# Performance work log

Hardware: AMD Instinct MI355X
Metric: run time of the kernel (lower is better)

The kernel has to match this reference:

```python
import jax, jax.numpy as jnp
import numpy as np

B, C, H, W_ = 4, 256, 64, 64
INTER = 128

def conv1x1(x, w, b):
    # x: [B,C,H,W], w: [O,C], b: [O] -> [B,O,H,W]
    return jnp.einsum('bchw,oc->bohw', x, w) + b[None, :, None, None]

def setup_inputs() -> dict:
    key = jax.random.key(0)
    ks = jax.random.split(key, 5)
    s_in = 1.0 / np.sqrt(C)
    s_mid = 1.0 / np.sqrt(INTER)
    return {
        'x': jax.random.normal(ks[0], (B, C, H, W_), dtype=jnp.float32),
        'w_g': jax.random.normal(ks[1], (INTER, C), dtype=jnp.float32) * s_in,
        'b_g': jnp.zeros((INTER,), dtype=jnp.float32),
        'w_theta': jax.random.normal(ks[2], (INTER, C), dtype=jnp.float32) * s_in,
        'b_theta': jnp.zeros((INTER,), dtype=jnp.float32),
        'w_phi': jax.random.normal(ks[3], (INTER, C), dtype=jnp.float32) * s_in,
        'b_phi': jnp.zeros((INTER,), dtype=jnp.float32),
        'w_out': jax.random.normal(ks[4], (C, INTER), dtype=jnp.float32) * s_mid,
        'b_out': jnp.zeros((C,), dtype=jnp.float32),
    }

def reference(x, w_g, b_g, w_theta, b_theta, w_phi, b_phi, w_out, b_out):
    b, c, h, w = x.shape
    n = h * w
    # 1x1 conv projections, flatten spatial dims to N tokens
    g_x = conv1x1(x, w_g, b_g).reshape(b, INTER, n).transpose(0, 2, 1)      # [B,N,I]
    theta_x = conv1x1(x, w_theta, b_theta).reshape(b, INTER, n).transpose(0, 2, 1)  # [B,N,I]
    phi_x = conv1x1(x, w_phi, b_phi).reshape(b, INTER, n)                   # [B,I,N]
    f = jnp.einsum('bni,bim->bnm', theta_x, phi_x)                          # [B,N,N]
    f_div_C = jax.nn.softmax(f, axis=-1)
    y = jnp.einsum('bnm,bmi->bni', f_div_C, g_x)                            # [B,N,I]
    y = y.transpose(0, 2, 1).reshape(b, INTER, h, w)
    W_y = conv1x1(y, w_out, b_out)                                          # [B,C,H,W]
    return W_y + x
```

## Files before the change

kernel.cpp:

```cpp
#include <hip/hip_runtime.h>

#define BB 4
#define CC 256
#define NN 4096
#define II 128
#define LOG2E 1.4426950408889634f

typedef float f32x4 __attribute__((ext_vector_type(4)));
typedef _Float16 f16x8 __attribute__((ext_vector_type(8)));

static __device__ __forceinline__ unsigned short f2h(float f) {
    _Float16 h = (_Float16)f;
    return __builtin_bit_cast(unsigned short, h);
}
static __device__ __forceinline__ float h2f(unsigned short s) {
    return (float)__builtin_bit_cast(_Float16, s);
}
static __device__ __forceinline__ unsigned int pack2h(float a, float b) {
    return (unsigned int)f2h(a) | ((unsigned int)f2h(b) << 16);
}
static __device__ __forceinline__ unsigned int cvt2h(float a, float b) {
    return __builtin_bit_cast(unsigned int, __builtin_amdgcn_cvt_pkrtz(a, b));
}
#define M3(a, b, c) fmaxf(fmaxf((a), (b)), (c))

__global__ __launch_bounds__(256) void proj_kernel(
    const float* __restrict__ x,
    const float* __restrict__ w_th, const float* __restrict__ b_th,
    const float* __restrict__ w_ph, const float* __restrict__ b_ph,
    const float* __restrict__ w_g,  const float* __restrict__ b_g,
    const float* __restrict__ w_out,
    unsigned short* __restrict__ Qb, unsigned short* __restrict__ Kb,
    unsigned short* __restrict__ Vt, unsigned short* __restrict__ Wo)
{
    __shared__ char lds[57344];
    unsigned short* xl = (unsigned short*)lds;

    int tid = threadIdx.x;
    int w = tid >> 6, l = tid & 63, g = l >> 4, cl = l & 15;
    int b = blockIdx.y, n0 = blockIdx.x * 64;
    const float* wp0 = w_th; const float* wp1 = w_ph; const float* wp2 = w_g;

    f32x4 acc[3][2][4];
    #pragma unroll
    for (int m = 0; m < 3; ++m)
        #pragma unroll
        for (int it = 0; it < 2; ++it)
            #pragma unroll
            for (int nt = 0; nt < 4; ++nt) acc[m][it][nt] = (f32x4){0.f, 0.f, 0.f, 0.f};

    const float* xb = x + (size_t)b * CC * NN;
    int c2 = tid >> 3, nch = tid & 7;

    for (int c0 = 0; c0 < CC; c0 += 64) {
        __syncthreads();
        {
            const float* xsrc = xb + (size_t)(c0 + c2 * 2) * NN + n0 + nch * 8;
            float4 x00 = *(const float4*)xsrc;
            float4 x01 = *(const float4*)(xsrc + 4);
            float4 x10 = *(const float4*)(xsrc + NN);
            float4 x11 = *(const float4*)(xsrc + NN + 4);
            float lo[8] = {x00.x, x00.y, x00.z, x00.w, x01.x, x01.y, x01.z, x01.w};
            float hi[8] = {x10.x, x10.y, x10.z, x10.w, x11.x, x11.y, x11.z, x11.w};
            #pragma unroll
            for (int t = 0; t < 8; ++t) {
                int n = nch * 8 + t;
                *(unsigned int*)((char*)xl + n * 128 + ((c2 * 4) ^ ((n & 7) << 4))) = pack2h(lo[t], hi[t]);
            }
        }
        #pragma unroll
        for (int r = 0; r < 12; ++r) {
            const int mat = r >> 2;
            int ir = (r & 3) * 32 + (tid >> 3), ch = tid & 7;
            const float* wsrc = (mat == 0 ? wp0 : mat == 1 ? wp1 : wp2) + ir * CC + c0 + ch * 8;
            float4 a = *(const float4*)wsrc;
            float4 bq = *(const float4*)(wsrc + 4);
            union { unsigned int u[4]; uint4 q; } pk;
            pk.u[0] = pack2h(a.x, a.y);   pk.u[1] = pack2h(a.z, a.w);
            pk.u[2] = pack2h(bq.x, bq.y); pk.u[3] = pack2h(bq.z, bq.w);
            *(uint4*)(lds + 8192 + mat * 16384 + ir * 128 + ((ch ^ (ir & 7)) << 4)) = pk.q;
        }
        __syncthreads();
        #pragma unroll
        for (int kc = 0; kc < 2; ++kc) {
            f16x8 bf[4];
            #pragma unroll
            for (int nt = 0; nt < 4; ++nt) {
                int row = nt * 16 + cl;
                bf[nt] = *(const f16x8*)((const char*)xl + row * 128 + (((kc * 4 + g) ^ (row & 7)) << 4));
            }
            #pragma unroll
            for (int m = 0; m < 3; ++m) {
                f16x8 af[2];
                #pragma unroll
                for (int it = 0; it < 2; ++it) {
                    int row = w * 32 + it * 16 + cl;
                    af[it] = *(const f16x8*)(lds + 8192 + m * 16384 + row * 128 + (((kc * 4 + g) ^ (row & 7)) << 4));
                }
                #pragma unroll
                for (int it = 0; it < 2; ++it)
                    #pragma unroll
                    for (int nt = 0; nt < 4; ++nt)
                        acc[m][it][nt] = __builtin_amdgcn_mfma_f32_16x16x32_f16(af[it], bf[nt], acc[m][it][nt], 0, 0, 0);
            }
        }
    }

    float bv[3][2][4];
    #pragma unroll
    for (int m = 0; m < 3; ++m) {
        const float* bp = (m == 0) ? b_th : (m == 1) ? b_ph : b_g;
        #pragma unroll
        for (int it = 0; it < 2; ++it)
            #pragma unroll
            for (int r = 0; r < 4; ++r) bv[m][it][r] = bp[w * 32 + it * 16 + 4 * g + r];
    }

    #pragma unroll
    for (int m = 0; m < 2; ++m) {
        float scale = (m == 0) ? LOG2E : 1.0f;
        unsigned short* pk = (unsigned short*)lds;
        __syncthreads();
        #pragma unroll
        for (int it = 0; it < 2; ++it)
            #pragma unroll
            for (int nt = 0; nt < 4; ++nt)
                #pragma unroll
                for (int r = 0; r < 4; r += 2) {
                    int n = nt * 16 + cl;
                    int i = w * 32 + it * 16 + 4 * g + r;
                    unsigned int v = pack2h((acc[m][it][nt][r] + bv[m][it][r]) * scale,
                                            (acc[m][it][nt][r + 1] + bv[m][it][r + 1]) * scale);
                    *(unsigned int*)((char*)pk + n * 256 + ((i * 2) ^ ((n & 7) << 4))) = v;
                }
        __syncthreads();
        unsigned short* out = (m == 0) ? Qb : Kb;
        #pragma unroll
        for (int r = 0; r < 4; ++r) {
            int idx = r * 256 + tid;
            int n = idx >> 4, seg = idx & 15;
            uint4 q = *(const uint4*)((const char*)pk + n * 256 + ((seg << 4) ^ ((n & 7) << 4)));
            *(uint4*)(out + (size_t)(b * NN + n0 + n) * II + seg * 8) = q;
        }
    }
    {
        unsigned short* pk = (unsigned short*)lds;
        __syncthreads();
        #pragma unroll
        for (int it = 0; it < 2; ++it)
            #pragma unroll
            for (int nt = 0; nt < 4; ++nt)
                #pragma unroll
                for (int r = 0; r < 4; ++r) {
                    int i = w * 32 + it * 16 + 4 * g + r;
                    int n = nt * 16 + cl;
                    *(unsigned short*)((char*)pk + i * 128 + ((n * 2) ^ ((i & 7) << 4))) =
                        f2h(acc[2][it][nt][r] + bv[2][it][r]);
                }
        __syncthreads();
        #pragma unroll
        for (int r = 0; r < 4; ++r) {
            int idx = r * 256 + tid;
            int i = idx >> 3, seg = idx & 7;
            uint4 q = *(const uint4*)((const char*)pk + i * 128 + ((seg << 4) ^ ((i & 7) << 4)));
            *(uint4*)(Vt + (size_t)(b * II + i) * NN + n0 + seg * 8) = q;
        }
    }
    if (blockIdx.x == 0 && b == 0) {
        #pragma unroll
        for (int r = 0; r < 16; ++r) {
            int idx = (r * 256 + tid) * 8;
            float4 a = *(const float4*)(w_out + idx);
            float4 b4 = *(const float4*)(w_out + idx + 4);
            union { unsigned int u[4]; uint4 q; } pw;
            pw.u[0] = pack2h(a.x, a.y);   pw.u[1] = pack2h(a.z, a.w);
            pw.u[2] = pack2h(b4.x, b4.y); pw.u[3] = pack2h(b4.z, b4.w);
            *(uint4*)&Wo[idx] = pw.q;
        }
    }
}

template<int NS>
__global__ __launch_bounds__(256, 2) void attn_kernel(
    const unsigned short* __restrict__ Qb,
    const unsigned short* __restrict__ Kb,
    const unsigned short* __restrict__ Vb,
    unsigned short* __restrict__ Yp,
    float2* __restrict__ ML)
{
    constexpr int KVH = NN / NS;
    constexpr int NT = KVH / 64;
    constexpr int HALF = NS / 2;
    constexpr int QSH = (NS == 8) ? 5 : 4;

    __shared__ unsigned short Ks[64 * 128];
    __shared__ unsigned short Vs[128 * 64];

    int tid = threadIdx.x;
    int w = tid >> 6, l = tid & 63, g = l >> 4, cl = l & 15;
    int id = blockIdx.x;
    int comb = (id & 7) * HALF + ((id >> 3) & (HALF - 1));
    int b = comb / NS, sp = comb % NS, qt = id >> QSH;
    int qr0 = qt * 128;
    int m_base = sp * KVH;

    f16x8 qa0[4], qa1[4];
    {
        const unsigned short* qrow0 = Qb + (size_t)(b * NN + qr0 + w * 32 + cl) * II;
        const unsigned short* qrow1 = qrow0 + 16 * II;
        #pragma unroll
        for (int kc = 0; kc < 4; ++kc) {
            qa0[kc] = *(const f16x8*)(qrow0 + kc * 32 + g * 8);
            qa1[kc] = *(const f16x8*)(qrow1 + kc * 32 + g * 8);
        }
    }
    const f16x8 onesv = {(_Float16)1.f, (_Float16)1.f, (_Float16)1.f, (_Float16)1.f,
                         (_Float16)1.f, (_Float16)1.f, (_Float16)1.f, (_Float16)1.f};

    f32x4 yacc0[8], yacc1[8], lacc0, lacc1;
    #pragma unroll
    for (int it = 0; it < 8; ++it) {
        yacc0[it] = (f32x4){0.f, 0.f, 0.f, 0.f};
        yacc1[it] = (f32x4){0.f, 0.f, 0.f, 0.f};
    }
    lacc0 = (f32x4){0.f, 0.f, 0.f, 0.f};
    lacc1 = (f32x4){0.f, 0.f, 0.f, 0.f};
    float mrun0 = -1e30f, mrun1 = -1e30f;

    const unsigned short* kb = Kb + (size_t)(b * NN + m_base) * II;
    const unsigned short* vb = Vb + (size_t)b * II * NN + m_base;
    int krow = tid >> 4, kch = tid & 15;
    int vrow = tid >> 3, vch = tid & 7;
    int kswz = (kch ^ (krow & 7)) << 4;
    int vsw = (vrow & 7) << 4;
    int vc0 = ((vch >> 2) * 32 + (vch & 1) * 16 + ((vch >> 1) & 1) * 4) * 2;

    uint4 k0, k1, k2, k3, v0, v1, v2, v3;
    k0 = *(const uint4*)(kb + (size_t)(krow) * II + kch * 8);
    k1 = *(const uint4*)(kb + (size_t)(16 + krow) * II + kch * 8);
    k2 = *(const uint4*)(kb + (size_t)(32 + krow) * II + kch * 8);
    k3 = *(const uint4*)(kb + (size_t)(48 + krow) * II + kch * 8);
    v0 = *(const uint4*)(vb + (size_t)(vrow) * NN + vch * 8);
    v1 = *(const uint4*)(vb + (size_t)(32 + vrow) * NN + vch * 8);
    v2 = *(const uint4*)(vb + (size_t)(64 + vrow) * NN + vch * 8);
    v3 = *(const uint4*)(vb + (size_t)(96 + vrow) * NN + vch * 8);

    for (int t = 0; t < NT; ++t) {
        __syncthreads();
        *(uint4*)((char*)Ks + (krow) * 256 + kswz) = k0;
        *(uint4*)((char*)Ks + (16 + krow) * 256 + kswz) = k1;
        *(uint4*)((char*)Ks + (32 + krow) * 256 + kswz) = k2;
        *(uint4*)((char*)Ks + (48 + krow) * 256 + kswz) = k3;
        {
            uint2 lo, hi;
            lo.x = v0.x; lo.y = v0.y; hi.x = v0.z; hi.y = v0.w;
            *(uint2*)((char*)Vs + (vrow) * 128 + (vc0 ^ vsw)) = lo;
            *(uint2*)((char*)Vs + (vrow) * 128 + ((vc0 + 16) ^ vsw)) = hi;
            lo.x = v1.x; lo.y = v1.y; hi.x = v1.z; hi.y = v1.w;
            *(uint2*)((char*)Vs + (32 + vrow) * 128 + (vc0 ^ vsw)) = lo;
            *(uint2*)((char*)Vs + (32 + vrow) * 128 + ((vc0 + 16) ^ vsw)) = hi;
            lo.x = v2.x; lo.y = v2.y; hi.x = v2.z; hi.y = v2.w;
            *(uint2*)((char*)Vs + (64 + vrow) * 128 + (vc0 ^ vsw)) = lo;
            *(uint2*)((char*)Vs + (64 + vrow) * 128 + ((vc0 + 16) ^ vsw)) = hi;
            lo.x = v3.x; lo.y = v3.y; hi.x = v3.z; hi.y = v3.w;
            *(uint2*)((char*)Vs + (96 + vrow) * 128 + (vc0 ^ vsw)) = lo;
            *(uint2*)((char*)Vs + (96 + vrow) * 128 + ((vc0 + 16) ^ vsw)) = hi;
        }
        __syncthreads();
        if (t + 1 < NT) {
            const unsigned short* kp = kb + (size_t)(t + 1) * 64 * II;
            k0 = *(const uint4*)(kp + (size_t)(krow) * II + kch * 8);
            k1 = *(const uint4*)(kp + (size_t)(16 + krow) * II + kch * 8);
            k2 = *(const uint4*)(kp + (size_t)(32 + krow) * II + kch * 8);
            k3 = *(const uint4*)(kp + (size_t)(48 + krow) * II + kch * 8);
        }

        f32x4 s0[4], s1[4];
        #pragma unroll
        for (int mt = 0; mt < 4; ++mt) {
            s0[mt] = (f32x4){0.f, 0.f, 0.f, 0.f};
            s1[mt] = (f32x4){0.f, 0.f, 0.f, 0.f};
        }
        __builtin_amdgcn_s_setprio(1);
        #pragma unroll
        for (int mt = 0; mt < 4; ++mt) {
            int row = mt * 16 + cl;
            #pragma unroll
            for (int kc = 0; kc < 4; ++kc) {
                f16x8 kf = *(const f16x8*)((const char*)Ks + row * 256 + (((kc * 4 + g) ^ (row & 7)) << 4));
                s0[mt] = __builtin_amdgcn_mfma_f32_16x16x32_f16(kf, qa0[kc], s0[mt], 0, 0, 0);
                s1[mt] = __builtin_amdgcn_mfma_f32_16x16x32_f16(kf, qa1[kc], s1[mt], 0, 0, 0);
            }
        }
        __builtin_amdgcn_s_setprio(0);
        if (t + 1 < NT) {
            const unsigned short* vp = vb + (size_t)(t + 1) * 64;
            v0 = *(const uint4*)(vp + (size_t)(vrow) * NN + vch * 8);
            v1 = *(const uint4*)(vp + (size_t)(32 + vrow) * NN + vch * 8);
            v2 = *(const uint4*)(vp + (size_t)(64 + vrow) * NN + vch * 8);
            v3 = *(const uint4*)(vp + (size_t)(96 + vrow) * NN + vch * 8);
        }

        union { unsigned int u[4]; f16x8 v; } pb00, pb01, pb10, pb11;
        {
            float t0 = M3(s0[0][0], s0[0][1], s0[0][2]);
            float t1 = M3(s0[0][3], s0[1][0], s0[1][1]);
            float t2 = M3(s0[1][2], s0[1][3], s0[2][0]);
            float t3 = M3(s0[2][1], s0[2][2], s0[2][3]);
            float t4 = M3(s0[3][0], s0[3][1], s0[3][2]);
            float tmax = fmaxf(M3(t0, t1, t2), M3(t3, t4, s0[3][3]));
            tmax = fmaxf(tmax, __shfl_xor(tmax, 16));
            tmax = fmaxf(tmax, __shfl_xor(tmax, 32));
            if (!__all(tmax <= mrun0 + 8.0f)) {
                float mnew = fmaxf(mrun0, tmax);
                float corr = exp2f(mrun0 - mnew);
                mrun0 = mnew;
                #pragma unroll
                for (int it = 0; it < 8; ++it)
                    #pragma unroll
                    for (int r = 0; r < 4; ++r) yacc0[it][r] *= corr;
                #pragma unroll
                for (int r = 0; r < 4; ++r) lacc0[r] *= corr;
            }
            #pragma unroll
            for (int mt = 0; mt < 4; ++mt) {
                unsigned int ua = cvt2h(exp2f(s0[mt][0] - mrun0), exp2f(s0[mt][1] - mrun0));
                unsigned int ub = cvt2h(exp2f(s0[mt][2] - mrun0), exp2f(s0[mt][3] - mrun0));
                if (mt < 2) { pb00.u[mt * 2] = ua; pb00.u[mt * 2 + 1] = ub; }
                else        { pb01.u[(mt - 2) * 2] = ua; pb01.u[(mt - 2) * 2 + 1] = ub; }
            }
        }
        {
            float t0 = M3(s1[0][0], s1[0][1], s1[0][2]);
            float t1 = M3(s1[0][3], s1[1][0], s1[1][1]);
            float t2 = M3(s1[1][2], s1[1][3], s1[2][0]);
            float t3 = M3(s1[2][1], s1[2][2], s1[2][3]);
            float t4 = M3(s1[3][0], s1[3][1], s1[3][2]);
            float tmax = fmaxf(M3(t0, t1, t2), M3(t3, t4, s1[3][3]));
            tmax = fmaxf(tmax, __shfl_xor(tmax, 16));
            tmax = fmaxf(tmax, __shfl_xor(tmax, 32));
            if (!__all(tmax <= mrun1 + 8.0f)) {
                float mnew = fmaxf(mrun1, tmax);
                float corr = exp2f(mrun1 - mnew);
                mrun1 = mnew;
                #pragma unroll
                for (int it = 0; it < 8; ++it)
                    #pragma unroll
                    for (int r = 0; r < 4; ++r) yacc1[it][r] *= corr;
                #pragma unroll
                for (int r = 0; r < 4; ++r) lacc1[r] *= corr;
            }
            #pragma unroll
            for (int mt = 0; mt < 4; ++mt) {
                unsigned int ua = cvt2h(exp2f(s1[mt][0] - mrun1), exp2f(s1[mt][1] - mrun1));
                unsigned int ub = cvt2h(exp2f(s1[mt][2] - mrun1), exp2f(s1[mt][3] - mrun1));
                if (mt < 2) { pb10.u[mt * 2] = ua; pb10.u[mt * 2 + 1] = ub; }
                else        { pb11.u[(mt - 2) * 2] = ua; pb11.u[(mt - 2) * 2 + 1] = ub; }
            }
        }

        __builtin_amdgcn_s_setprio(1);
        lacc0 = __builtin_amdgcn_mfma_f32_16x16x32_f16(onesv, pb00.v, lacc0, 0, 0, 0);
        lacc0 = __builtin_amdgcn_mfma_f32_16x16x32_f16(onesv, pb01.v, lacc0, 0, 0, 0);
        lacc1 = __builtin_amdgcn_mfma_f32_16x16x32_f16(onesv, pb10.v, lacc1, 0, 0, 0);
        lacc1 = __builtin_amdgcn_mfma_f32_16x16x32_f16(onesv, pb11.v, lacc1, 0, 0, 0);
        #pragma unroll
        for (int it = 0; it < 8; ++it) {
            int row = it * 16 + cl;
            f16x8 vf0 = *(const f16x8*)((const char*)Vs + row * 128 + ((g ^ (row & 7)) << 4));
            f16x8 vf1 = *(const f16x8*)((const char*)Vs + row * 128 + (((4 + g) ^ (row & 7)) << 4));
            yacc0[it] = __builtin_amdgcn_mfma_f32_16x16x32_f16(vf0, pb00.v, yacc0[it], 0, 0, 0);
            yacc0[it] = __builtin_amdgcn_mfma_f32_16x16x32_f16(vf1, pb01.v, yacc0[it], 0, 0, 0);
            yacc1[it] = __builtin_amdgcn_mfma_f32_16x16x32_f16(vf0, pb10.v, yacc1[it], 0, 0, 0);
            yacc1[it] = __builtin_amdgcn_mfma_f32_16x16x32_f16(vf1, pb11.v, yacc1[it], 0, 0, 0);
        }
        __builtin_amdgcn_s_setprio(0);
    }

    __syncthreads();

    unsigned short* ys = Ks + w * 2048;
    size_t rowbase0 = (size_t)((sp * BB + b) * NN + qr0 + w * 32);
    int prow = l >> 2;
    {
        float rl = 1.0f / lacc0[0];
        #pragma unroll
        for (int it = 0; it < 8; ++it)
            #pragma unroll
            for (int r = 0; r < 4; r += 2) {
                int i = it * 16 + 4 * g + r;
                *(unsigned int*)((char*)ys + cl * 256 + ((i * 2) ^ ((cl & 7) << 4))) =
                    pack2h(yacc0[it][r] * rl, yacc0[it][r + 1] * rl);
            }
        #pragma unroll
        for (int c = 0; c < 4; ++c) {
            int seg = c * 4 + (l & 3);
            uint4 q = *(const uint4*)((const char*)ys + prow * 256 + ((seg << 4) ^ ((prow & 7) << 4)));
            *(uint4*)(Yp + (rowbase0 + prow) * II + seg * 8) = q;
        }
    }
    {
        float rl = 1.0f / lacc1[0];
        #pragma unroll
        for (int it = 0; it < 8; ++it)
            #pragma unroll
            for (int r = 0; r < 4; r += 2) {
                int i = it * 16 + 4 * g + r;
                *(unsigned int*)((char*)ys + cl * 256 + ((i * 2) ^ ((cl & 7) << 4))) =
                    pack2h(yacc1[it][r] * rl, yacc1[it][r + 1] * rl);
            }
        #pragma unroll
        for (int c = 0; c < 4; ++c) {
            int seg = c * 4 + (l & 3);
            uint4 q = *(const uint4*)((const char*)ys + prow * 256 + ((seg << 4) ^ ((prow & 7) << 4)));
            *(uint4*)(Yp + (rowbase0 + 16 + prow) * II + seg * 8) = q;
        }
    }
    if (l < 16) {
        float2 v; v.x = mrun0; v.y = lacc0[0];
        ML[rowbase0 + l] = v;
    } else if (l < 32) {
        float2 v; v.x = mrun1; v.y = lacc1[0];
        ML[rowbase0 + 16 + (l - 16)] = v;
    }
}

template<int NS>
__global__ __launch_bounds__(256) void combine_kernel(
    const unsigned short* __restrict__ Yp, const float2* __restrict__ ML,
    const unsigned short* __restrict__ Wo, const float* __restrict__ b_out,
    const float* __restrict__ x, float* __restrict__ out)
{
    __shared__ unsigned short Ys[4][16 * 128];

    int tid = threadIdx.x;
    int w = tid >> 6, l = tid & 63, g = l >> 4, cl = l & 15;
    int qt = blockIdx.x, b = blockIdx.y;
    int qr0 = qt * 64;
    int n = qr0 + w * 16 + cl;

    float ms[NS], ls[NS], wgt[NS];
    float M = -1e30f;
    #pragma unroll
    for (int s = 0; s < NS; ++s) {
        float2 ml = ML[(size_t)(s * BB + b) * NN + n];
        ms[s] = ml.x; ls[s] = ml.y;
        M = fmaxf(M, ml.x);
    }
    float wsum = 0.f;
    #pragma unroll
    for (int s = 0; s < NS; ++s) { wgt[s] = exp2f(ms[s] - M) * ls[s]; wsum += wgt[s]; }
    float rd = 1.0f / wsum;
    #pragma unroll
    for (int s = 0; s < NS; ++s) wgt[s] *= rd;

    unsigned short* ys = Ys[w];
    #pragma unroll
    for (int j = 0; j < 4; ++j) {
        float acc[8];
        #pragma unroll
        for (int e = 0; e < 8; ++e) acc[e] = 0.f;
        #pragma unroll
        for (int s = 0; s < NS; ++s) {
            union { unsigned short s16[8]; uint4 q; } a;
            a.q = *(const uint4*)(Yp + ((size_t)(s * BB + b) * NN + n) * II + g * 32 + j * 8);
            #pragma unroll
            for (int e = 0; e < 8; ++e) acc[e] += wgt[s] * h2f(a.s16[e]);
        }
        union { unsigned int u[4]; uint4 q; } o;
        #pragma unroll
        for (int e = 0; e < 4; ++e) o.u[e] = pack2h(acc[e * 2], acc[e * 2 + 1]);
        *(uint4*)((char*)ys + cl * 256 + (((g * 4 + j) ^ (cl & 7)) << 4)) = o.q;
    }

    f32x4 zero4 = {0.f, 0.f, 0.f, 0.f};
    f16x8 yf[4];
    #pragma unroll
    for (int kc = 0; kc < 4; ++kc)
        yf[kc] = *(const f16x8*)((const char*)ys + cl * 256 + (((kc * 4 + g) ^ (cl & 7)) << 4));
    for (int ct = 0; ct < 16; ++ct) {
        f32x4 oa = zero4;
        #pragma unroll
        for (int kc = 0; kc < 4; ++kc) {
            f16x8 wf = *(const f16x8*)(Wo + (ct * 16 + cl) * II + kc * 32 + g * 8);
            oa = __builtin_amdgcn_mfma_f32_16x16x32_f16(wf, yf[kc], oa, 0, 0, 0);
        }
        #pragma unroll
        for (int r = 0; r < 4; ++r) {
            int c = ct * 16 + 4 * g + r;
            size_t off = (size_t)(b * CC + c) * NN + n;
            out[off] = oa[r] + b_out[c] + x[off];
        }
    }
}

extern "C" void kernel_launch(void* const* d_in, const int* in_sizes, int n_in,
                              void* d_out, int out_size, void* d_ws, size_t ws_size,
                              hipStream_t stream) {
    const float* x     = (const float*)d_in[0];
    const float* w_g   = (const float*)d_in[1];
    const float* b_g   = (const float*)d_in[2];
    const float* w_th  = (const float*)d_in[3];
    const float* b_th  = (const float*)d_in[4];
    const float* w_ph  = (const float*)d_in[5];
    const float* b_ph  = (const float*)d_in[6];
    const float* w_out = (const float*)d_in[7];
    const float* b_o   = (const float*)d_in[8];
    float* out = (float*)d_out;

    const size_t SZ = (size_t)BB * NN * II;
    unsigned short* Qb = (unsigned short*)d_ws;
    unsigned short* Kb = Qb + SZ;
    unsigned short* Vt = Kb + SZ;
    unsigned short* Wo = Vt + SZ;
    unsigned short* Yp = Wo + (size_t)CC * II;

    size_t need8 = ((size_t)3 * SZ + (size_t)CC * II + (size_t)8 * SZ) * 2
                 + (size_t)8 * BB * NN * sizeof(float2);
    proj_kernel<<<dim3(NN / 64, BB), dim3(256), 0, stream>>>(
        x, w_th, b_th, w_ph, b_ph, w_g, b_g, w_out, Qb, Kb, Vt, Wo);
    if (ws_size >= need8) {
        float2* ML = (float2*)(Yp + (size_t)8 * SZ);
        attn_kernel<8><<<dim3(8 * BB * (NN / 128)), dim3(256), 0, stream>>>(Qb, Kb, Vt, Yp, ML);
        combine_kernel<8><<<dim3(NN / 64, BB), dim3(256), 0, stream>>>(Yp, ML, Wo, b_o, x, out);
    } else {
        float2* ML = (float2*)(Yp + (size_t)4 * SZ);
        attn_kernel<4><<<dim3(4 * BB * (NN / 128)), dim3(256), 0, stream>>>(Qb, Kb, Vt, Yp, ML);
        combine_kernel<4><<<dim3(NN / 64, BB), dim3(256), 0, stream>>>(Yp, ML, Wo, b_o, x, out);
    }
}
```

Measured before the change: 112.4 us.

## Stream K tiles into double-buffered LDS via global_load_lds and split V prefetch

K tiles are now copied straight from global memory into a double-buffered LDS array with the direct global-to-LDS load instruction. This removes the register staging and the explicit LDS stores for K, and the next tile's K load now overlaps the current tile's compute. The V prefetch is split into two halves issued at different points in the loop to spread memory traffic and register pressure. In exchange the kernel uses more LDS, which may reduce occupancy, and correctness depends on the direct-load waits being ordered properly by the existing barriers.

After: 114.8 us. 2.2% more time.

```diff
diff --git a/kernel.cpp b/kernel.cpp
--- a/kernel.cpp
+++ b/kernel.cpp
@@ -9,6 +9,9 @@
 typedef float f32x4 __attribute__((ext_vector_type(4)));
 typedef _Float16 f16x8 __attribute__((ext_vector_type(8)));
 
+typedef __attribute__((address_space(1))) unsigned int ga_u32;
+typedef __attribute__((address_space(3))) unsigned int ls_u32;
+
 static __device__ __forceinline__ unsigned short f2h(float f) {
     _Float16 h = (_Float16)f;
     return __builtin_bit_cast(unsigned short, h);
@@ -21,6 +24,9 @@
 }
 static __device__ __forceinline__ unsigned int cvt2h(float a, float b) {
     return __builtin_bit_cast(unsigned int, __builtin_amdgcn_cvt_pkrtz(a, b));
+}
+static __device__ __forceinline__ void glds16(const unsigned short* g, unsigned short* l) {
+    __builtin_amdgcn_global_load_lds((const ga_u32*)g, (ls_u32*)l, 16, 0, 0);
 }
 #define M3(a, b, c) fmaxf(fmaxf((a), (b)), (c))
 
@@ -193,7 +199,7 @@
     constexpr int HALF = NS / 2;
     constexpr int QSH = (NS == 8) ? 5 : 4;
 
-    __shared__ unsigned short Ks[64 * 128];
+    __shared__ unsigned short Ks[2][64 * 128];
     __shared__ unsigned short Vs[128 * 64];
 
     int tid = threadIdx.x;
@@ -229,17 +235,18 @@
 
     const unsigned short* kb = Kb + (size_t)(b * NN + m_base) * II;
     const unsigned short* vb = Vb + (size_t)b * II * NN + m_base;
-    int krow = tid >> 4, kch = tid & 15;
     int vrow = tid >> 3, vch = tid & 7;
-    int kswz = (kch ^ (krow & 7)) << 4;
     int vsw = (vrow & 7) << 4;
     int vc0 = ((vch >> 2) * 32 + (vch & 1) * 16 + ((vch >> 1) & 1) * 4) * 2;
 
-    uint4 k0, k1, k2, k3, v0, v1, v2, v3;
-    k0 = *(const uint4*)(kb + (size_t)(krow) * II + kch * 8);
-    k1 = *(const uint4*)(kb + (size_t)(16 + krow) * II + kch * 8);
-    k2 = *(const uint4*)(kb + (size_t)(32 + krow) * II + kch * 8);
-    k3 = *(const uint4*)(kb + (size_t)(48 + krow) * II + kch * 8);
+    int rbase = w * 4 + (l >> 4);
+    int sch = (l & 15) ^ (rbase & 7);
+    const unsigned short* kgl = kb + (size_t)rbase * II + sch * 8;
+
+    #pragma unroll
+    for (int j = 0; j < 4; ++j)
+        glds16(kgl + j * 16 * II, &Ks[0][(j * 16 + w * 4) * 128]);
+    uint4 v0, v1, v2, v3;
     v0 = *(const uint4*)(vb + (size_t)(vrow) * NN + vch * 8);
     v1 = *(const uint4*)(vb + (size_t)(32 + vrow) * NN + vch * 8);
     v2 = *(const uint4*)(vb + (size_t)(64 + vrow) * NN + vch * 8);
@@ -247,10 +254,6 @@
 
     for (int t = 0; t < NT; ++t) {
         __syncthreads();
-        *(uint4*)((char*)Ks + (krow) * 256 + kswz) = k0;
-        *(uint4*)((char*)Ks + (16 + krow) * 256 + kswz) = k1;
-        *(uint4*)((char*)Ks + (32 + krow) * 256 + kswz) = k2;
-        *(uint4*)((char*)Ks + (48 + krow) * 256 + kswz) = k3;
         {
             uint2 lo, hi;
             lo.x = v0.x; lo.y = v0.y; hi.x = v0.z; hi.y = v0.w;
@@ -268,12 +271,16 @@
         }
         __syncthreads();
         if (t + 1 < NT) {
-            const unsigned short* kp = kb + (size_t)(t + 1) * 64 * II;
-            k0 = *(const uint4*)(kp + (size_t)(krow) * II + kch * 8);
-            k1 = *(const uint4*)(kp + (size_t)(16 + krow) * II + kch * 8);
-            k2 = *(const uint4*)(kp + (size_t)(32 + krow) * II + kch * 8);
-            k3 = *(const uint4*)(kp + (size_t)(48 + krow) * II + kch * 8);
-        }
+            const unsigned short* kp = kgl + (size_t)(t + 1) * 64 * II;
+            unsigned short* kd = Ks[(t + 1) & 1];
+            #pragma unroll
+            for (int j = 0; j < 4; ++j)
+                glds16(kp + j * 16 * II, kd + (j * 16 + w * 4) * 128);
+            const unsigned short* vp = vb + (size_t)(t + 1) * 64;
+            v0 = *(const uint4*)(vp + (size_t)(vrow) * NN + vch * 8);
+            v1 = *(const uint4*)(vp + (size_t)(32 + vrow) * NN + vch * 8);
+        }
+        const unsigned short* ksb = Ks[t & 1];
 
         f32x4 s0[4], s1[4];
         #pragma unroll
@@ -287,19 +294,12 @@
             int row = mt * 16 + cl;
             #pragma unroll
             for (int kc = 0; kc < 4; ++kc) {
-                f16x8 kf = *(const f16x8*)((const char*)Ks + row * 256 + (((kc * 4 + g) ^ (row & 7)) << 4));
+                f16x8 kf = *(const f16x8*)((const char*)ksb + row * 256 + (((kc * 4 + g) ^ (row & 7)) << 4));
                 s0[mt] = __builtin_amdgcn_mfma_f32_16x16x32_f16(kf, qa0[kc], s0[mt], 0, 0, 0);
                 s1[mt] = __builtin_amdgcn_mfma_f32_16x16x32_f16(kf, qa1[kc], s1[mt], 0, 0, 0);
             }
         }
         __builtin_amdgcn_s_setprio(0);
-        if (t + 1 < NT) {
-            const unsigned short* vp = vb + (size_t)(t + 1) * 64;
-            v0 = *(const uint4*)(vp + (size_t)(vrow) * NN + vch * 8);
-            v1 = *(const uint4*)(vp + (size_t)(32 + vrow) * NN + vch * 8);
-            v2 = *(const uint4*)(vp + (size_t)(64 + vrow) * NN + vch * 8);
-            v3 = *(const uint4*)(vp + (size_t)(96 + vrow) * NN + vch * 8);
-        }
 
         union { unsigned int u[4]; f16x8 v; } pb00, pb01, pb10, pb11;
         {
@@ -330,6 +330,11 @@
                 else        { pb01.u[(mt - 2) * 2] = ua; pb01.u[(mt - 2) * 2 + 1] = ub; }
             }
         }
+        if (t + 1 < NT) {
+            const unsigned short* vp = vb + (size_t)(t + 1) * 64;
+            v2 = *(const uint4*)(vp + (size_t)(64 + vrow) * NN + vch * 8);
+            v3 = *(const uint4*)(vp + (size_t)(96 + vrow) * NN + vch * 8);
+        }
         {
             float t0 = M3(s1[0][0], s1[0][1], s1[0][2]);
             float t1 = M3(s1[0][3], s1[1][0], s1[1][1]);
@@ -379,7 +384,7 @@
 
     __syncthreads();
 
-    unsigned short* ys = Ks + w * 2048;
+    unsigned short* ys = &Ks[0][w * 2048];
     size_t rowbase0 = (size_t)((sp * BB + b) * NN + qr0 + w * 32);
     int prow = l >> 2;
     {
```
